# Kernel tuning notes

Hardware: AMD Instinct MI355X
Metric: run time of the kernel (lower is better)

## Reference

```python
import jax, jax.numpy as jnp
import numpy as np

EMBED_DIM = 1024
NUM_HEADS = 16
HEAD_DIM = EMBED_DIM // NUM_HEADS
LN_EPS = 1e-12
B, S = 2, 2048


def setup_inputs() -> dict:
    key = jax.random.key(0)
    ks = jax.random.split(key, 12)
    scale = 1.0 / np.sqrt(EMBED_DIM)
    d = EMBED_DIM
    return {
        "in_features": jax.random.normal(ks[0], (B, S, d), dtype=jnp.float32),
        "tgt_mask": jnp.ones((B, S), dtype=jnp.float32),
        "Wq": jax.random.normal(ks[1], (d, d), dtype=jnp.float32) * scale,
        "bq": jnp.zeros((d,), dtype=jnp.float32),
        "Wk": jax.random.normal(ks[2], (d, d), dtype=jnp.float32) * scale,
        "bk": jnp.zeros((d,), dtype=jnp.float32),
        "Wv": jax.random.normal(ks[3], (d, d), dtype=jnp.float32) * scale,
        "bv": jnp.zeros((d,), dtype=jnp.float32),
        "Wo": jax.random.normal(ks[4], (d, d), dtype=jnp.float32) * scale,
        "bo": jnp.zeros((d,), dtype=jnp.float32),
        "gamma": jnp.ones((d,), dtype=jnp.float32),
        "beta": jnp.zeros((d,), dtype=jnp.float32),
    }


def _split_heads(x):  # [B,S,D] -> [B,H,S,Dh]
    b, s, _ = x.shape
    return x.reshape(b, s, NUM_HEADS, HEAD_DIM).transpose(0, 2, 1, 3)


def reference(in_features, tgt_mask, Wq, bq, Wk, bk, Wv, bv, Wo, bo, gamma, beta):
    # Self-attention (tgt_features defaults to in_features). Dropout in eval mode (identity).
    q = _split_heads(in_features @ Wq.T + bq)
    k = _split_heads(in_features @ Wk.T + bk)
    v = _split_heads(in_features @ Wv.T + bv)
    # scores: [B,H,S,S]
    scores = jnp.einsum("bhqd,bhkd->bhqk", q, k) / jnp.sqrt(jnp.float32(HEAD_DIM))
    scores = scores + (1.0 - tgt_mask)[:, None, None, :] * (-100000.0)
    attn = jax.nn.softmax(scores, axis=-1)
    ctx = jnp.einsum("bhqk,bhkd->bhqd", attn, v)  # [B,H,S,Dh]
    ctx = ctx.transpose(0, 2, 1, 3).reshape(in_features.shape)  # merge heads
    out = ctx @ Wo.T + bo
    x = out + in_features
    mu = jnp.mean(x, axis=-1, keepdims=True)
    var = jnp.mean(jnp.square(x - mu), axis=-1, keepdims=True)
    return (x - mu) / jnp.sqrt(var + LN_EPS) * gamma + beta
```

## Files before the change

kernel.cpp:

```cpp
#include <hip/hip_runtime.h>
#include <hip/hip_bf16.h>

#define DM   1024
#define HEADS 16
#define DH    64
#define SEQ  2048
#define BATCH   2
#define LOG2E 1.44269504088896f

typedef __attribute__((ext_vector_type(8))) short short8;
typedef __attribute__((ext_vector_type(4))) short bf16x4;
typedef __attribute__((ext_vector_type(4))) float floatx4;
typedef __attribute__((ext_vector_type(16))) float floatx16;

__device__ __forceinline__ short f2b(float f) {
    union { float f; unsigned u; } v; v.f = f;
    unsigned r = v.u + 0x7FFFu + ((v.u >> 16) & 1u);
    return (short)(r >> 16);
}

#if __has_builtin(__builtin_amdgcn_exp2f)
__device__ __forceinline__ float fexp2(float x) { return __builtin_amdgcn_exp2f(x); }
#else
__device__ __forceinline__ float fexp2(float x) { return exp2f(x); }
#endif

__device__ __forceinline__ void async_copy16(const short* gsrc, short* ldst) {
    __builtin_amdgcn_global_load_lds(
        (const __attribute__((address_space(1))) void*)gsrc,
        (__attribute__((address_space(3))) void*)ldst,
        16, 0, 0);
}

__global__ __launch_bounds__(256) void cvt_all(const float* __restrict__ x,
        const float* __restrict__ wq, const float* __restrict__ wk,
        const float* __restrict__ wv, const float* __restrict__ wo,
        const float* __restrict__ mask,
        short* __restrict__ xb, short* __restrict__ wqkv, short* __restrict__ wob,
        float* __restrict__ maddg)
{
    const int b = blockIdx.x;
    if (b >= 8192) {
        const int bb = b - 8192;
        const float* mrow = mask + (size_t)bb * SEQ;
        float* mg = maddg + (size_t)bb * SEQ;
#pragma unroll
        for (int i = 0; i < 8; ++i) {
            const int idx = threadIdx.x * 8 + i;
            mg[idx] = (1.f - mrow[idx]) * (-100000.f * LOG2E);
        }
        return;
    }
    const float* src; short* dst; int idx;
    if (b < 4096)      { src = x;  dst = xb;                idx = b; }
    else if (b < 5120) { src = wq; dst = wqkv;              idx = b - 4096; }
    else if (b < 6144) { src = wk; dst = wqkv + (1 << 20);  idx = b - 5120; }
    else if (b < 7168) { src = wv; dst = wqkv + (2 << 20);  idx = b - 6144; }
    else               { src = wo; dst = wob;               idx = b - 7168; }
    const int i = idx * 256 + threadIdx.x;
    floatx4 v = ((const floatx4*)src)[i];
    bf16x4 o;
    o.x = f2b(v.x); o.y = f2b(v.y); o.z = f2b(v.z); o.w = f2b(v.w);
    ((bf16x4*)dst)[i] = o;
}

__global__ __launch_bounds__(256) void gemm_qkv(const short* __restrict__ A,
        const short* __restrict__ B,
        const float* __restrict__ bq, const float* __restrict__ bk,
        const float* __restrict__ bv,
        short* __restrict__ qw, short* __restrict__ kw, short* __restrict__ vw)
{
    __shared__ short As[128 * 32];
    __shared__ short Bs[128 * 32];
    const int m0 = blockIdx.x * 128, n0 = blockIdx.y * 128;
    const int w = threadIdx.x >> 6, lane = threadIdx.x & 63;
    const int l16 = lane & 15, quad = lane >> 4;
    const int wm = w >> 1, wn = w & 1;
    const int lr = lane >> 2, lc = (lane & 3) * 8;

    floatx4 acc[4][4];
#pragma unroll
    for (int i = 0; i < 4; ++i)
#pragma unroll
        for (int j = 0; j < 4; ++j) acc[i][j] = (floatx4){0.f, 0.f, 0.f, 0.f};

    for (int kt = 0; kt < DM / 32; ++kt) {
        const int k0 = kt * 32;
        __syncthreads();
        async_copy16(A + (size_t)(m0 + w * 32 + lr) * DM + k0 + lc,      &As[w * 1024]);
        async_copy16(A + (size_t)(m0 + w * 32 + 16 + lr) * DM + k0 + lc, &As[w * 1024 + 512]);
        async_copy16(B + (size_t)(n0 + w * 32 + lr) * DM + k0 + lc,      &Bs[w * 1024]);
        async_copy16(B + (size_t)(n0 + w * 32 + 16 + lr) * DM + k0 + lc, &Bs[w * 1024 + 512]);
        __syncthreads();

        short8 af[4], bf[4];
#pragma unroll
        for (int i = 0; i < 4; ++i)
            af[i] = *(const short8*)&As[(wm * 64 + i * 16 + l16) * 32 + quad * 8];
#pragma unroll
        for (int j = 0; j < 4; ++j)
            bf[j] = *(const short8*)&Bs[(wn * 64 + j * 16 + l16) * 32 + quad * 8];
#pragma unroll
        for (int i = 0; i < 4; ++i)
#pragma unroll
            for (int j = 0; j < 4; ++j)
                acc[i][j] = __builtin_amdgcn_mfma_f32_16x16x32_bf16(af[i], bf[j], acc[i][j], 0, 0, 0);
    }

    const int m_base = m0 + wm * 64 + quad * 4;
#pragma unroll
    for (int j = 0; j < 4; ++j) {
        const int nb = n0 + wn * 64 + j * 16;
        const int t = nb >> 10;
        const int nn = (nb & 1023) + l16;
        const int h = nn >> 6, dh = nn & 63;
        const float* bias = (t == 0) ? bq : (t == 1) ? bk : bv;
        short* dst = (t == 0) ? qw : (t == 1) ? kw : vw;
        const float mulf = (t == 0) ? (0.125f * LOG2E) : 1.0f;
        const float bvv = bias[nn];
#pragma unroll
        for (int i = 0; i < 4; ++i)
#pragma unroll
            for (int r = 0; r < 4; ++r) {
                const int m = m_base + i * 16 + r;
                const int b = m >> 11, s = m & (SEQ - 1);
                dst[(((size_t)(b * HEADS + h)) * SEQ + s) * DH + dh] =
                    f2b((acc[i][j][r] + bvv) * mulf);
            }
    }
}

__global__ __launch_bounds__(256) void transpose_v(const short* __restrict__ v,
                                                   short* __restrict__ vt)
{
    __shared__ short tl[64][72];
    const int st = blockIdx.x;
    const int bh = blockIdx.y;
    const int t = threadIdx.x;
    const int row = t >> 2, off = (t & 3) * 16;
    const short* vp = v + ((size_t)bh * SEQ + st * 64 + row) * DH + off;
    *(short8*)&tl[row][off]     = *(const short8*)vp;
    *(short8*)&tl[row][off + 8] = *(const short8*)(vp + 8);
    __syncthreads();
    short8 o0, o1;
#pragma unroll
    for (int j = 0; j < 8; ++j) { o0[j] = tl[off + j][row]; o1[j] = tl[off + 8 + j][row]; }
    short* op = vt + ((size_t)bh * DH + row) * SEQ + st * 64 + off;
    *(short8*)op = o0;
    *(short8*)(op + 8) = o1;
}

__global__ __launch_bounds__(256) void attn_kernel(const short* __restrict__ q,
        const short* __restrict__ k, const short* __restrict__ vt,
        const float* __restrict__ maddg, short* __restrict__ ctx)
{
    const int id    = blockIdx.x;
    const int qtile = id >> 5;
    const int bh    = id & 31;
    const int bidx  = bh >> 4;
    const int wave = threadIdx.x >> 6, lane = threadIdx.x & 63;
    const int l32 = lane & 31, half = lane >> 5;
    const int kw = wave & 1, qw = wave >> 1;

    __shared__ __align__(16) short smem[20480];
    short* p_lds    = smem + 12288;
    float* mask_lds = (float*)(smem + 16384);
    short* Ct       = smem;
    float* l_fin    = (float*)(smem + 4608);

    const short* kbase0 = k  + (size_t)bh * SEQ * DH;
    const short* vbase0 = vt + (size_t)bh * DH * SEQ;
    const float* mrow   = maddg + (size_t)bidx * SEQ;

    const int qrow = qtile * 64 + qw * 32 + l32;
    const short* qbase = q + ((size_t)bh * SEQ + qrow) * DH;
    short8 b_q[4];
#pragma unroll
    for (int kk = 0; kk < 4; ++kk)
        b_q[kk] = *(const short8*)(qbase + kk * 16 + half * 8);

    floatx16 oacc;
#pragma unroll
    for (int r = 0; r < 16; ++r) oacc[r] = 0.f;
    float l_run = 0.f;

    int srw[2], gg[2];
#pragma unroll
    for (int i = 0; i < 2; ++i) {
        const int slot = i * 256 + wave * 64 + lane;
        srw[i] = slot >> 3;
        gg[i]  = (slot & 7) ^ (srw[i] & 7);
    }

    const int prow = qw * 32 + l32;

    auto stage_k = [&](int buf, int kt) {
        const short* kbase = kbase0 + (size_t)(kt * 64) * DH;
        const int ko = buf << 12;
#pragma unroll
        for (int i = 0; i < 2; ++i)
            async_copy16(kbase + srw[i] * DH + gg[i] * 8,
                         &smem[ko + (i * 256 + wave * 64) * 8]);
    };
    auto stage_v = [&](int kt) {
        const short* vbase = vbase0 + kt * 64;
#pragma unroll
        for (int i = 0; i < 2; ++i)
            async_copy16(vbase + (size_t)srw[i] * SEQ + gg[i] * 8,
                         &smem[8192 + (i * 256 + wave * 64) * 8]);
    };

#pragma unroll
    for (int i = 0; i < 2; ++i)
        async_copy16((const short*)mrow + (i * 256 + threadIdx.x) * 8,
                     &smem[16384 + (i * 256 + wave * 64) * 8]);
    stage_k(0, 0);

    int cur = 0;
    for (int kt = 0; kt < SEQ / 64; ++kt) {
        asm volatile("" ::: "memory");
        __builtin_amdgcn_s_barrier();

        floatx4 md[4];
#pragma unroll
        for (int g = 0; g < 4; ++g)
            md[g] = *(const floatx4*)&mask_lds[kt * 64 + kw * 32 + 8 * g + 4 * half];

        stage_v(kt);
        __builtin_amdgcn_sched_barrier(0);
        const bool has_next = (kt + 1 < SEQ / 64);
        if (has_next) {
            stage_k(cur ^ 1, kt + 1);
            asm volatile("s_waitcnt vmcnt(4)" ::: "memory");
        } else {
            asm volatile("s_waitcnt vmcnt(2)" ::: "memory");
        }
        __builtin_amdgcn_s_barrier();

        floatx16 s;
#pragma unroll
        for (int g = 0; g < 4; ++g)
#pragma unroll
            for (int r = 0; r < 4; ++r) s[g * 4 + r] = md[g][r];
        {
            const int ko = cur << 12;
            const int krow = kw * 32 + l32;
            const int ksw = krow & 7;
#pragma unroll
            for (int kk = 0; kk < 4; ++kk) {
                const int c = kk * 2 + half;
                short8 a = *(const short8*)&smem[ko + krow * 64 + ((c ^ ksw) * 8)];
                s = __builtin_amdgcn_mfma_f32_32x32x16_bf16(a, b_q[kk], s, 0, 0, 0);
            }
        }

        float lsum = 0.f;
        const int psw = prow & 7;
#pragma unroll
        for (int g = 0; g < 4; ++g) {
            const float p0 = fexp2(fminf(s[g * 4 + 0], 40.f));
            const float p1 = fexp2(fminf(s[g * 4 + 1], 40.f));
            const float p2 = fexp2(fminf(s[g * 4 + 2], 40.f));
            const float p3 = fexp2(fminf(s[g * 4 + 3], 40.f));
            lsum += (p0 + p1) + (p2 + p3);
            union { __hip_bfloat162 h[2]; bf16x4 v; } u;
            u.h[0] = __float22bfloat162_rn(make_float2(p0, p1));
            u.h[1] = __float22bfloat162_rn(make_float2(p2, p3));
            const int c = kw * 4 + g;
            *(bf16x4*)&p_lds[prow * 64 + ((c ^ psw) * 8) + 4 * half] = u.v;
        }
        l_run += lsum;

        asm volatile("s_waitcnt lgkmcnt(0)" ::: "memory");
        if (has_next) {
            asm volatile("s_waitcnt vmcnt(2)" ::: "memory");
        } else {
            asm volatile("s_waitcnt vmcnt(0)" ::: "memory");
        }
        __builtin_amdgcn_s_barrier();

        {
            const int vrow = kw * 32 + l32;
            const int vsw = vrow & 7;
#pragma unroll
            for (int kk = 0; kk < 4; ++kk) {
                const int c = kk * 2 + half;
                short8 av = *(const short8*)&smem[8192 + vrow * 64 + ((c ^ vsw) * 8)];
                short8 bp = *(const short8*)&p_lds[prow * 64 + ((c ^ psw) * 8)];
                oacc = __builtin_amdgcn_mfma_f32_32x32x16_bf16(av, bp, oacc, 0, 0, 0);
            }
        }
        cur ^= 1;
    }

    asm volatile("" ::: "memory");
    __builtin_amdgcn_s_barrier();

    const float l_mine = l_run + __shfl_xor(l_run, 32);
    l_fin[kw * 64 + prow] = l_mine;
    asm volatile("s_waitcnt lgkmcnt(0)" ::: "memory");
    __builtin_amdgcn_s_barrier();

    const int h = bh & 15, bb = bh >> 4;
    const float rl = 1.f / (l_fin[prow] + l_fin[64 + prow]);
#pragma unroll
    for (int g = 0; g < 4; ++g) {
        bf16x4 p;
        p.x = f2b(oacc[g * 4 + 0] * rl);
        p.y = f2b(oacc[g * 4 + 1] * rl);
        p.z = f2b(oacc[g * 4 + 2] * rl);
        p.w = f2b(oacc[g * 4 + 3] * rl);
        const int dh = kw * 32 + 8 * g + 4 * half;
        *(bf16x4*)&Ct[prow * 72 + dh] = p;
    }
    __syncthreads();
    {
        const int row = threadIdx.x >> 2, ch = threadIdx.x & 3;
        short8 v0 = *(const short8*)&Ct[row * 72 + ch * 16];
        short8 v1 = *(const short8*)&Ct[row * 72 + ch * 16 + 8];
        short* gp = ctx + ((size_t)(bb * SEQ + qtile * 64 + row)) * DM + h * 64 + ch * 16;
        *(short8*)gp = v0;
        *(short8*)(gp + 8) = v1;
    }
}

__global__ __launch_bounds__(256) void gemm_o(const short* __restrict__ A,
        const short* __restrict__ B, const float* __restrict__ bo,
        const float* __restrict__ xin, float* __restrict__ out)
{
    __shared__ short As[128 * 32];
    __shared__ short Bs[64 * 32];
    const int m0 = blockIdx.x * 128, n0 = blockIdx.y * 64;
    const int w = threadIdx.x >> 6, lane = threadIdx.x & 63;
    const int l16 = lane & 15, quad = lane >> 4;
    const int wm = w >> 1, wn = w & 1;

    floatx4 acc[4][2];
#pragma unroll
    for (int i = 0; i < 4; ++i)
#pragma unroll
        for (int j = 0; j < 2; ++j) acc[i][j] = (floatx4){0.f, 0.f, 0.f, 0.f};

    const int c0 = w * 64 + lane;

    for (int kt = 0; kt < DM / 32; ++kt) {
        const int k0 = kt * 32;
        __syncthreads();
        {
            const int ra0 = c0 >> 2,          ca0 = (c0 & 3) * 8;
            const int ra1 = (256 + c0) >> 2,  ca1 = (c0 & 3) * 8;
            async_copy16(A + (size_t)(m0 + ra0) * DM + k0 + ca0, &As[(w * 64) * 8]);
            async_copy16(A + (size_t)(m0 + ra1) * DM + k0 + ca1, &As[(256 + w * 64) * 8]);
            const int rb = c0 >> 2, cb = (c0 & 3) * 8;
            async_copy16(B + (size_t)(n0 + rb) * DM + k0 + cb,   &Bs[(w * 64) * 8]);
        }
        __syncthreads();

        short8 af[4], bf[2];
#pragma unroll
        for (int i = 0; i < 4; ++i)
            af[i] = *(const short8*)&As[(wm * 64 + i * 16 + l16) * 32 + quad * 8];
#pragma unroll
        for (int j = 0; j < 2; ++j)
            bf[j] = *(const short8*)&Bs[(wn * 32 + j * 16 + l16) * 32 + quad * 8];
#pragma unroll
        for (int i = 0; i < 4; ++i)
#pragma unroll
            for (int j = 0; j < 2; ++j)
                acc[i][j] = __builtin_amdgcn_mfma_f32_16x16x32_bf16(af[i], bf[j], acc[i][j], 0, 0, 0);
    }

    const int m_base = m0 + wm * 64 + quad * 4;
#pragma unroll
    for (int j = 0; j < 2; ++j) {
        const int n = n0 + wn * 32 + j * 16 + l16;
        const float bvv = bo[n];
#pragma unroll
        for (int i = 0; i < 4; ++i)
#pragma unroll
            for (int r = 0; r < 4; ++r) {
                const int m = m_base + i * 16 + r;
                const size_t idx = (size_t)m * DM + n;
                out[idx] = acc[i][j][r] + bvv + xin[idx];
            }
    }
}

__global__ __launch_bounds__(256) void ln_kernel(float* __restrict__ y,
        const float* __restrict__ gamma, const float* __restrict__ beta)
{
    const int row = blockIdx.x;
    const int t = threadIdx.x;
    const int wave = t >> 6, lane = t & 63;
    const floatx4 v = ((const floatx4*)(y + (size_t)row * DM))[t];
    float s  = v.x + v.y + v.z + v.w;
    float q2 = v.x * v.x + v.y * v.y + v.z * v.z + v.w * v.w;
#pragma unroll
    for (int off = 1; off < 64; off <<= 1) {
        s  += __shfl_xor(s, off);
        q2 += __shfl_xor(q2, off);
    }
    __shared__ float rs[4], rq[4];
    if (lane == 0) { rs[wave] = s; rq[wave] = q2; }
    __syncthreads();
    const float S  = rs[0] + rs[1] + rs[2] + rs[3];
    const float Q2 = rq[0] + rq[1] + rq[2] + rq[3];
    const float mu = S * (1.f / DM);
    float var = Q2 * (1.f / DM) - mu * mu;
    var = fmaxf(var, 0.f);
    const float rstd = rsqrtf(var + 1e-12f);
    const floatx4 g = ((const floatx4*)gamma)[t];
    const floatx4 bt = ((const floatx4*)beta)[t];
    floatx4 o;
    o.x = (v.x - mu) * rstd * g.x + bt.x;
    o.y = (v.y - mu) * rstd * g.y + bt.y;
    o.z = (v.z - mu) * rstd * g.z + bt.z;
    o.w = (v.w - mu) * rstd * g.w + bt.w;
    ((floatx4*)(y + (size_t)row * DM))[t] = o;
}

extern "C" void kernel_launch(void* const* d_in, const int* in_sizes, int n_in,
                              void* d_out, int out_size, void* d_ws, size_t ws_size,
                              hipStream_t stream) {
    const float* x     = (const float*)d_in[0];
    const float* mask  = (const float*)d_in[1];
    const float* Wq    = (const float*)d_in[2];
    const float* bq    = (const float*)d_in[3];
    const float* Wk    = (const float*)d_in[4];
    const float* bk    = (const float*)d_in[5];
    const float* Wv    = (const float*)d_in[6];
    const float* bv    = (const float*)d_in[7];
    const float* Wo    = (const float*)d_in[8];
    const float* bo    = (const float*)d_in[9];
    const float* gamma = (const float*)d_in[10];
    const float* beta  = (const float*)d_in[11];
    float* out = (float*)d_out;

    const size_t NTOK = (size_t)BATCH * SEQ * DM;
    const size_t WSZ  = (size_t)DM * DM;
    short* xb   = (short*)d_ws;
    short* wqkv = xb + NTOK;
    short* wob  = wqkv + 3 * WSZ;
    short* qw   = wob + WSZ;
    short* kw   = qw + NTOK;
    short* vw   = kw + NTOK;
    short* vtw  = vw + NTOK;
    short* ctxw = vw;
    float* maddg = (float*)(vtw + NTOK);

    dim3 blk(256);
    cvt_all<<<dim3(8194), blk, 0, stream>>>(x, Wq, Wk, Wv, Wo, mask, xb, wqkv, wob, maddg);
    gemm_qkv<<<dim3(32, 24), blk, 0, stream>>>(xb, wqkv, bq, bk, bv, qw, kw, vw);
    transpose_v<<<dim3(SEQ / 64, BATCH * HEADS), blk, 0, stream>>>(vw, vtw);
    attn_kernel<<<dim3(32 * 32), blk, 0, stream>>>(qw, kw, vtw, maddg, ctxw);
    gemm_o<<<dim3(32, 16), blk, 0, stream>>>(ctxw, wob, bo, x, out);
    ln_kernel<<<BATCH * SEQ, blk, 0, stream>>>(out, gamma, beta);
}
```

Baseline: 217.1 us.

## Double-buffer LDS tiles in QKV and output-projection GEMMs to overlap loads

Both GEMM kernels now keep two shared-memory stages and prefetch the next K-tile with async copies while MFMAs run on the current one. Partial vmcnt waits hold back only the loads for the tile about to be consumed, so the new prefetch stays in flight. The aim is to hide global-load latency that the old load-sync-compute loop exposed. It doubles LDS use per block, which may lower occupancy, and it relies on hand-written waitcnt counts matching the copies issued per stage.

```diff
diff --git a/kernel.cpp b/kernel.cpp
--- a/kernel.cpp
+++ b/kernel.cpp
@@ -70,8 +70,8 @@
         const float* __restrict__ bv,
         short* __restrict__ qw, short* __restrict__ kw, short* __restrict__ vw)
 {
-    __shared__ short As[128 * 32];
-    __shared__ short Bs[128 * 32];
+    __shared__ __align__(16) short As[2][128 * 32];
+    __shared__ __align__(16) short Bs[2][128 * 32];
     const int m0 = blockIdx.x * 128, n0 = blockIdx.y * 128;
     const int w = threadIdx.x >> 6, lane = threadIdx.x & 63;
     const int l16 = lane & 15, quad = lane >> 4;
@@ -84,27 +84,41 @@
 #pragma unroll
         for (int j = 0; j < 4; ++j) acc[i][j] = (floatx4){0.f, 0.f, 0.f, 0.f};
 
+    auto stage = [&](int buf, int kt) {
+        const int k0 = kt * 32;
+        async_copy16(A + (size_t)(m0 + w * 32 + lr) * DM + k0 + lc,      &As[buf][w * 1024]);
+        async_copy16(A + (size_t)(m0 + w * 32 + 16 + lr) * DM + k0 + lc, &As[buf][w * 1024 + 512]);
+        async_copy16(B + (size_t)(n0 + w * 32 + lr) * DM + k0 + lc,      &Bs[buf][w * 1024]);
+        async_copy16(B + (size_t)(n0 + w * 32 + 16 + lr) * DM + k0 + lc, &Bs[buf][w * 1024 + 512]);
+    };
+
+    stage(0, 0);
+    int cur = 0;
     for (int kt = 0; kt < DM / 32; ++kt) {
-        const int k0 = kt * 32;
-        __syncthreads();
-        async_copy16(A + (size_t)(m0 + w * 32 + lr) * DM + k0 + lc,      &As[w * 1024]);
-        async_copy16(A + (size_t)(m0 + w * 32 + 16 + lr) * DM + k0 + lc, &As[w * 1024 + 512]);
-        async_copy16(B + (size_t)(n0 + w * 32 + lr) * DM + k0 + lc,      &Bs[w * 1024]);
-        async_copy16(B + (size_t)(n0 + w * 32 + 16 + lr) * DM + k0 + lc, &Bs[w * 1024 + 512]);
-        __syncthreads();
+        asm volatile("" ::: "memory");
+        __builtin_amdgcn_s_barrier();
+
+        if (kt + 1 < DM / 32) {
+            stage(cur ^ 1, kt + 1);
+            asm volatile("s_waitcnt vmcnt(4)" ::: "memory");
+        } else {
+            asm volatile("s_waitcnt vmcnt(0)" ::: "memory");
+        }
+        __builtin_amdgcn_s_barrier();
 
         short8 af[4], bf[4];
 #pragma unroll
         for (int i = 0; i < 4; ++i)
-            af[i] = *(const short8*)&As[(wm * 64 + i * 16 + l16) * 32 + quad * 8];
+            af[i] = *(const short8*)&As[cur][(wm * 64 + i * 16 + l16) * 32 + quad * 8];
 #pragma unroll
         for (int j = 0; j < 4; ++j)
-            bf[j] = *(const short8*)&Bs[(wn * 64 + j * 16 + l16) * 32 + quad * 8];
+            bf[j] = *(const short8*)&Bs[cur][(wn * 64 + j * 16 + l16) * 32 + quad * 8];
 #pragma unroll
         for (int i = 0; i < 4; ++i)
 #pragma unroll
             for (int j = 0; j < 4; ++j)
                 acc[i][j] = __builtin_amdgcn_mfma_f32_16x16x32_bf16(af[i], bf[j], acc[i][j], 0, 0, 0);
+        cur ^= 1;
     }
 
     const int m_base = m0 + wm * 64 + quad * 4;
@@ -328,8 +342,8 @@
         const short* __restrict__ B, const float* __restrict__ bo,
         const float* __restrict__ xin, float* __restrict__ out)
 {
-    __shared__ short As[128 * 32];
-    __shared__ short Bs[64 * 32];
+    __shared__ __align__(16) short As[2][128 * 32];
+    __shared__ __align__(16) short Bs[2][64 * 32];
     const int m0 = blockIdx.x * 128, n0 = blockIdx.y * 64;
     const int w = threadIdx.x >> 6, lane = threadIdx.x & 63;
     const int l16 = lane & 15, quad = lane >> 4;
@@ -343,31 +357,43 @@
 
     const int c0 = w * 64 + lane;
 
+    auto stage = [&](int buf, int kt) {
+        const int k0 = kt * 32;
+        const int ra0 = c0 >> 2,          ca0 = (c0 & 3) * 8;
+        const int ra1 = (256 + c0) >> 2,  ca1 = (c0 & 3) * 8;
+        async_copy16(A + (size_t)(m0 + ra0) * DM + k0 + ca0, &As[buf][(w * 64) * 8]);
+        async_copy16(A + (size_t)(m0 + ra1) * DM + k0 + ca1, &As[buf][(256 + w * 64) * 8]);
+        const int rb = c0 >> 2, cb = (c0 & 3) * 8;
+        async_copy16(B + (size_t)(n0 + rb) * DM + k0 + cb,   &Bs[buf][(w * 64) * 8]);
+    };
+
+    stage(0, 0);
+    int cur = 0;
     for (int kt = 0; kt < DM / 32; ++kt) {
-        const int k0 = kt * 32;
-        __syncthreads();
-        {
-            const int ra0 = c0 >> 2,          ca0 = (c0 & 3) * 8;
-            const int ra1 = (256 + c0) >> 2,  ca1 = (c0 & 3) * 8;
-            async_copy16(A + (size_t)(m0 + ra0) * DM + k0 + ca0, &As[(w * 64) * 8]);
-            async_copy16(A + (size_t)(m0 + ra1) * DM + k0 + ca1, &As[(256 + w * 64) * 8]);
-            const int rb = c0 >> 2, cb = (c0 & 3) * 8;
-            async_copy16(B + (size_t)(n0 + rb) * DM + k0 + cb,   &Bs[(w * 64) * 8]);
-        }
-        __syncthreads();
+        asm volatile("" ::: "memory");
+        __builtin_amdgcn_s_barrier();
+
+        if (kt + 1 < DM / 32) {
+            stage(cur ^ 1, kt + 1);
+            asm volatile("s_waitcnt vmcnt(3)" ::: "memory");
+        } else {
+            asm volatile("s_waitcnt vmcnt(0)" ::: "memory");
+        }
+        __builtin_amdgcn_s_barrier();
 
         short8 af[4], bf[2];
 #pragma unroll
         for (int i = 0; i < 4; ++i)
-            af[i] = *(const short8*)&As[(wm * 64 + i * 16 + l16) * 32 + quad * 8];
+            af[i] = *(const short8*)&As[cur][(wm * 64 + i * 16 + l16) * 32 + quad * 8];
 #pragma unroll
         for (int j = 0; j < 2; ++j)
-            bf[j] = *(const short8*)&Bs[(wn * 32 + j * 16 + l16) * 32 + quad * 8];
+            bf[j] = *(const short8*)&Bs[cur][(wn * 32 + j * 16 + l16) * 32 + quad * 8];
 #pragma unroll
         for (int i = 0; i < 4; ++i)
 #pragma unroll
             for (int j = 0; j < 2; ++j)
                 acc[i][j] = __builtin_amdgcn_mfma_f32_16x16x32_bf16(af[i], bf[j], acc[i][j], 0, 0, 0);
+        cur ^= 1;
     }
 
     const int m_base = m0 + wm * 64 + quad * 4;
```

Result: slower. 225.0 us (+3.6%).
